# Kernel tuning notes

Measured on AMD Instinct MI355X. Metric: run time of the kernel, lower is better.

## Reference

```python
import jax, jax.numpy as jnp
import numpy as np

HEADS = 8
DIM_HEAD = 32
SCALE = DIM_HEAD ** -0.5


def setup_inputs() -> dict:
    key = jax.random.key(0)
    k1, k2, k3 = jax.random.split(key, 3)
    B, H, W, C = 16, 64, 64, 256
    hidden = HEADS * DIM_HEAD  # 256
    x = jax.random.normal(k1, (B, H, W, C), dtype=jnp.float32)
    # 1x1 convs with no bias == dense matmuls over channel dim (glorot-ish scale)
    w_qkv = jax.random.normal(k2, (C, 3 * hidden), dtype=jnp.float32) * (1.0 / np.sqrt(C))
    w_out = jax.random.normal(k3, (hidden, C), dtype=jnp.float32) * (1.0 / np.sqrt(hidden))
    return {"x": x, "w_qkv": w_qkv, "w_out": w_out}


def reference(x, w_qkv, w_out):
    B, H, W, C = x.shape
    n = H * W
    # to_qkv: 1x1 conv, no bias
    qkv = jnp.einsum('bhwc,cf->bhwf', x, w_qkv)  # [B,H,W,3*hidden]
    q, k, v = jnp.split(qkv, 3, axis=-1)

    def to_heads(t):
        # 'b x y (h c) -> b h c (x y)'
        t = t.reshape(B, n, HEADS, DIM_HEAD)
        return jnp.transpose(t, (0, 2, 3, 1))  # [B, heads, dim_head, n]

    q, k, v = to_heads(q), to_heads(k), to_heads(v)
    q = jax.nn.softmax(q, axis=-2) * SCALE      # softmax over feature dim d
    k = jax.nn.softmax(k, axis=-1)              # softmax over spatial dim n
    context = jnp.einsum('bhdn,bhen->bhde', k, v)   # [B, heads, d, e]
    out = jnp.einsum('bhde,bhdn->bhen', context, q)  # [B, heads, e, n]
    # 'b h c (x y) -> b x y (h c)'
    out = jnp.transpose(out, (0, 3, 1, 2)).reshape(B, H, W, HEADS * DIM_HEAD)
    # to_out: 1x1 conv, no bias
    return jnp.einsum('bhwf,fc->bhwc', out, w_out)
```

## Files before the change

### kernel.cpp

```cpp
#include <hip/hip_runtime.h>

using short8 = __attribute__((ext_vector_type(8))) short;
using f32x4  = __attribute__((ext_vector_type(4))) float;

#define SCALE_Q 0.17677669529663687f
#define NCHUNK 16

__device__ __forceinline__ unsigned short f2bf(float f) {
  unsigned u = __float_as_uint(f);
  return (unsigned short)((u + 0x7FFFu + ((u >> 16) & 1u)) >> 16);
}
__device__ __forceinline__ float bf2f(unsigned h) { return __uint_as_float(h << 16); }

__device__ __forceinline__ void bf8_to_f(uint4 r, float* o) {
  o[0] = bf2f(r.x & 0xffffu); o[1] = bf2f(r.x >> 16);
  o[2] = bf2f(r.y & 0xffffu); o[3] = bf2f(r.y >> 16);
  o[4] = bf2f(r.z & 0xffffu); o[5] = bf2f(r.z >> 16);
  o[6] = bf2f(r.w & 0xffffu); o[7] = bf2f(r.w >> 16);
}
__device__ __forceinline__ unsigned pack2(float a, float b) {
  return (unsigned)f2bf(a) | ((unsigned)f2bf(b) << 16);
}

__global__ __launch_bounds__(256) void prep_kernel(
    const float* __restrict__ x, const float* __restrict__ wqkv, const float* __restrict__ wout,
    unsigned short* __restrict__ xb, unsigned short* __restrict__ wqkvT,
    unsigned short* __restrict__ woutT) {
  const int blk = blockIdx.x;
  if (blk < 16384) {
    const size_t i = ((size_t)blk * 256 + threadIdx.x) * 4;
    const float4 v = *(const float4*)(x + i);
    *(ushort4*)(xb + i) = make_ushort4(f2bf(v.x), f2bf(v.y), f2bf(v.z), f2bf(v.w));
  } else if (blk < 16384 + 768) {
    const int n = blk - 16384, k = threadIdx.x;
    wqkvT[n * 256 + k] = f2bf(wqkv[(size_t)k * 768 + n]);
  } else {
    const int c = blk - 16384 - 768, f = threadIdx.x;
    woutT[c * 256 + f] = f2bf(wout[(size_t)f * 256 + c]);
  }
}

template <typename OutT>
__global__ __launch_bounds__(256) void gemm_bt(
    const unsigned short* __restrict__ A, const unsigned short* __restrict__ BT,
    OutT* __restrict__ D, int M, int N, int K,
    size_t strideA, size_t strideB, size_t strideD) {
  __shared__ unsigned short As[128][40];
  __shared__ unsigned short Bs[128][40];
  const int bn = blockIdx.x, bm = blockIdx.y, bz = blockIdx.z;
  const int tid = threadIdx.x, lane = tid & 63, wid = tid >> 6;
  const int wr = wid >> 1, wc = wid & 1;
  const int fr = lane & 15, fk = (lane >> 4) * 8;
  f32x4 acc[4][4] = {};
  const size_t abase = (size_t)bz * strideA + (size_t)bm * 128 * K;
  const size_t bbase = (size_t)bz * strideB + (size_t)bn * 128 * K;

  for (int kt = 0; kt < K; kt += 32) {
    for (int c = tid; c < 512; c += 256) {
      const int row = c >> 2, kc = (c & 3) * 8;
      *(uint4*)&As[row][kc] = *(const uint4*)(A + abase + (size_t)row * K + kt + kc);
      *(uint4*)&Bs[row][kc] = *(const uint4*)(BT + bbase + (size_t)row * K + kt + kc);
    }
    __syncthreads();
    short8 af[4], bfr[4];
#pragma unroll
    for (int i = 0; i < 4; ++i) {
      af[i]  = *(const short8*)&As[wr * 64 + i * 16 + fr][fk];
      bfr[i] = *(const short8*)&Bs[wc * 64 + i * 16 + fr][fk];
    }
#pragma unroll
    for (int mi = 0; mi < 4; ++mi)
#pragma unroll
      for (int nj = 0; nj < 4; ++nj)
        acc[mi][nj] = __builtin_amdgcn_mfma_f32_16x16x32_bf16(af[mi], bfr[nj], acc[mi][nj], 0, 0, 0);
    __syncthreads();
  }
  const size_t r0 = (size_t)bm * 128 + wr * 64;
  const int c0 = bn * 128 + wc * 64;
  OutT* Dz = D + (size_t)bz * strideD;
#pragma unroll
  for (int mi = 0; mi < 4; ++mi)
#pragma unroll
    for (int nj = 0; nj < 4; ++nj) {
      const int col = c0 + nj * 16 + fr;
#pragma unroll
      for (int r = 0; r < 4; ++r) {
        const size_t row = r0 + mi * 16 + (lane >> 4) * 4 + r;
        const float v = acc[mi][nj][r];
        if constexpr (sizeof(OutT) == 2) Dz[row * N + col] = (OutT)f2bf(v);
        else                             Dz[row * N + col] = v;
      }
    }
}

__global__ __launch_bounds__(256) void ctx_part_kernel(const unsigned short* __restrict__ qkv,
                                                       float* __restrict__ part,
                                                       float* __restrict__ spart) {
  const int blk = blockIdx.x;
  const int bh = blk >> 4, chunk = blk & 15;
  const int b = bh >> 3, h = bh & 7;
  const int tid = threadIdx.x, d = tid & 31, g = tid >> 5;
  const unsigned short* kbase =
      qkv + (size_t)b * 4096 * 768 + 256 + h * 32 + (size_t)chunk * 256 * 768;
  const unsigned short* vbase = kbase + 256;

  __shared__ float ek[64][36], vv[64][36];
  float a0 = 0.f, a1 = 0.f, a2 = 0.f, a3 = 0.f, ssum = 0.f;
  const int e0 = g * 4;
  const int sn = tid >> 2, sc = (tid & 3) * 8;
  const unsigned short* kp0 = kbase + (size_t)sn * 768 + sc;
  const unsigned short* vp0 = vbase + (size_t)sn * 768 + sc;
  uint4 kr = *(const uint4*)kp0;
  uint4 vr = *(const uint4*)vp0;
  for (int n0 = 0; n0 < 256; n0 += 64) {
    float kf[8], vf[8];
    bf8_to_f(kr, kf); bf8_to_f(vr, vf);
    uint4 krn = kr, vrn = vr;
    if (n0 + 64 < 256) {
      krn = *(const uint4*)(kp0 + (size_t)(n0 + 64) * 768);
      vrn = *(const uint4*)(vp0 + (size_t)(n0 + 64) * 768);
    }
#pragma unroll
    for (int j = 0; j < 8; ++j) { ek[sn][sc + j] = __expf(kf[j]); vv[sn][sc + j] = vf[j]; }
    __syncthreads();
#pragma unroll 8
    for (int i = 0; i < 64; ++i) {
      const float kd = ek[i][d];
      const float4 v4 = *(const float4*)&vv[i][e0];
      ssum += kd;
      a0 += kd * v4.x; a1 += kd * v4.y; a2 += kd * v4.z; a3 += kd * v4.w;
    }
    __syncthreads();
    kr = krn; vr = vrn;
  }
  float* pp = part + ((size_t)chunk * 128 + bh) * 1024 + d * 32 + e0;
  pp[0] = a0; pp[1] = a1; pp[2] = a2; pp[3] = a3;
  if (g == 0) spart[((size_t)chunk * 128 + bh) * 32 + d] = ssum;
}

__global__ __launch_bounds__(256) void ctx_combine_kernel(const float* __restrict__ part,
                                                          const float* __restrict__ spart,
                                                          float* __restrict__ ctx) {
  const int bh = blockIdx.x, tid = threadIdx.x;
  __shared__ float sinv[32];
  if (tid < 32) {
    float s = 0.f;
#pragma unroll
    for (int c = 0; c < NCHUNK; ++c) s += spart[((size_t)c * 128 + bh) * 32 + tid];
    sinv[tid] = 1.0f / s;
  }
  __syncthreads();
  float4 acc = make_float4(0.f, 0.f, 0.f, 0.f);
#pragma unroll
  for (int c = 0; c < NCHUNK; ++c) {
    const float4 p = *(const float4*)(part + ((size_t)c * 128 + bh) * 1024 + tid * 4);
    acc.x += p.x; acc.y += p.y; acc.z += p.z; acc.w += p.w;
  }
  const float si = sinv[tid >> 3];
  float4* cp = (float4*)(ctx + (size_t)bh * 1024 + tid * 4);
  *cp = make_float4(acc.x * si, acc.y * si, acc.z * si, acc.w * si);
}

__global__ __launch_bounds__(256) void qsoftmax_kernel(const unsigned short* __restrict__ qkv,
                                                       unsigned short* __restrict__ qs) {
  const size_t t = (size_t)blockIdx.x * 256 + threadIdx.x;
  const size_t n = t >> 3; const int h = (int)(t & 7);
  const unsigned short* qp = qkv + n * 768 + h * 32;
  float q[32];
  bf8_to_f(*(const uint4*)(qp + 0),  q + 0);
  bf8_to_f(*(const uint4*)(qp + 8),  q + 8);
  bf8_to_f(*(const uint4*)(qp + 16), q + 16);
  bf8_to_f(*(const uint4*)(qp + 24), q + 24);
  float mx = q[0];
#pragma unroll
  for (int j = 1; j < 32; ++j) mx = fmaxf(mx, q[j]);
  float ssum = 0.f;
#pragma unroll
  for (int j = 0; j < 32; ++j) { q[j] = __expf(q[j] - mx); ssum += q[j]; }
  const float inv = SCALE_Q / ssum;
  uint4* op = (uint4*)(qs + n * 256 + h * 32);
  op[0] = make_uint4(pack2(q[0]*inv,  q[1]*inv),  pack2(q[2]*inv,  q[3]*inv),
                     pack2(q[4]*inv,  q[5]*inv),  pack2(q[6]*inv,  q[7]*inv));
  op[1] = make_uint4(pack2(q[8]*inv,  q[9]*inv),  pack2(q[10]*inv, q[11]*inv),
                     pack2(q[12]*inv, q[13]*inv), pack2(q[14]*inv, q[15]*inv));
  op[2] = make_uint4(pack2(q[16]*inv, q[17]*inv), pack2(q[18]*inv, q[19]*inv),
                     pack2(q[20]*inv, q[21]*inv), pack2(q[22]*inv, q[23]*inv));
  op[3] = make_uint4(pack2(q[24]*inv, q[25]*inv), pack2(q[26]*inv, q[27]*inv),
                     pack2(q[28]*inv, q[29]*inv), pack2(q[30]*inv, q[31]*inv));
}

__global__ __launch_bounds__(256) void w2_kernel(const float* __restrict__ ctx,
                                                 const unsigned short* __restrict__ woutT,
                                                 unsigned short* __restrict__ W2T) {
  const int b = blockIdx.x >> 4, cg = blockIdx.x & 15;
  const int tid = threadIdx.x;
  __shared__ float cs[8 * 32 * 32];
  {
    const float4* src = (const float4*)(ctx + (size_t)b * 8192);
    float4* dst = (float4*)cs;
#pragma unroll
    for (int i = 0; i < 8; ++i) dst[tid + i * 256] = src[tid + i * 256];
  }
  __syncthreads();
  const int c = cg * 16 + (tid >> 4), chunk = tid & 15;
  const int h = chunk >> 1, d0 = (chunk & 1) * 16;
  float wf[32];
  {
    const uint4* wp = (const uint4*)(woutT + (size_t)c * 256 + h * 32);
    bf8_to_f(wp[0], wf + 0); bf8_to_f(wp[1], wf + 8);
    bf8_to_f(wp[2], wf + 16); bf8_to_f(wp[3], wf + 24);
  }
  unsigned short o[16];
#pragma unroll
  for (int dd = 0; dd < 16; ++dd) {
    const float* cp = cs + h * 1024 + (d0 + dd) * 32;
    float acc = 0.f;
#pragma unroll
    for (int e = 0; e < 32; ++e) acc += cp[e] * wf[e];
    o[dd] = f2bf(acc);
  }
  uint4* op = (uint4*)(W2T + ((size_t)b * 256 + c) * 256 + chunk * 16);
  op[0] = make_uint4((unsigned)o[0] | ((unsigned)o[1] << 16), (unsigned)o[2] | ((unsigned)o[3] << 16),
                     (unsigned)o[4] | ((unsigned)o[5] << 16), (unsigned)o[6] | ((unsigned)o[7] << 16));
  op[1] = make_uint4((unsigned)o[8] | ((unsigned)o[9] << 16), (unsigned)o[10] | ((unsigned)o[11] << 16),
                     (unsigned)o[12] | ((unsigned)o[13] << 16), (unsigned)o[14] | ((unsigned)o[15] << 16));
}

extern "C" void kernel_launch(void* const* d_in, const int* in_sizes, int n_in,
                              void* d_out, int out_size, void* d_ws, size_t ws_size,
                              hipStream_t stream) {
  const float* x     = (const float*)d_in[0];
  const float* wqkv  = (const float*)d_in[1];
  const float* wout  = (const float*)d_in[2];
  float* out = (float*)d_out;

  char* ws = (char*)d_ws;
  unsigned short* xb    = (unsigned short*)(ws);
  unsigned short* wqkvT = (unsigned short*)(ws + 33554432);
  unsigned short* woutT = (unsigned short*)(ws + 33947648);
  unsigned short* qkv   = (unsigned short*)(ws + 34078720);
  float*          ctx   = (float*)        (ws + 134742016);
  unsigned short* qs    = (unsigned short*)(ws + 135266304);
  float*          part  = (float*)(ws);
  float*          spart = (float*)(ws + 8388608);
  unsigned short* W2T   = (unsigned short*)(ws + 12582912);

  prep_kernel<<<16384 + 768 + 256, 256, 0, stream>>>(x, wqkv, wout, xb, wqkvT, woutT);
  gemm_bt<unsigned short><<<dim3(6, 512, 1), 256, 0, stream>>>(
      xb, wqkvT, qkv, 65536, 768, 256, 0, 0, 0);
  ctx_part_kernel<<<2048, 256, 0, stream>>>(qkv, part, spart);
  ctx_combine_kernel<<<128, 256, 0, stream>>>(part, spart, ctx);
  qsoftmax_kernel<<<2048, 256, 0, stream>>>(qkv, qs);
  w2_kernel<<<256, 256, 0, stream>>>(ctx, woutT, W2T);
  gemm_bt<float><<<dim3(2, 32, 16), 256, 0, stream>>>(
      qs, W2T, out, 4096, 256, 256, 4096 * 256, 256 * 256, 4096 * 256);
}
```

Baseline: 184.9 us.

## Fuse Q softmax into QKV GEMM epilogue and use direct global-to-LDS loads

The QKV projection GEMM now applies the per-head feature softmax to the Q columns in its epilogue, using lane shuffles, and writes bf16 Q straight to the qs buffer. The separate qsoftmax kernel is removed, and the intermediate buffer shrinks to K/V only, which saves a write and re-read of Q. The GEMM mainloop now uses global_load_lds with a 64-wide K tile and an unpadded LDS layout, plus a blockwise grid swizzle for better cache locality. The unpadded LDS rows may cause bank conflicts on the fragment reads.

```diff
diff --git a/kernel.cpp b/kernel.cpp
--- a/kernel.cpp
+++ b/kernel.cpp
@@ -18,8 +18,11 @@
   o[4] = bf2f(r.z & 0xffffu); o[5] = bf2f(r.z >> 16);
   o[6] = bf2f(r.w & 0xffffu); o[7] = bf2f(r.w >> 16);
 }
-__device__ __forceinline__ unsigned pack2(float a, float b) {
-  return (unsigned)f2bf(a) | ((unsigned)f2bf(b) << 16);
+
+__device__ __forceinline__ void gl_lds16(const unsigned short* g, unsigned short* l) {
+  __builtin_amdgcn_global_load_lds(
+      (const __attribute__((address_space(1))) void*)g,
+      (__attribute__((address_space(3))) void*)l, 16, 0, 0);
 }
 
 __global__ __launch_bounds__(256) void prep_kernel(
@@ -40,52 +43,92 @@
   }
 }
 
-template <typename OutT>
+template <typename OutT, bool QSOFT, bool SWZ>
 __global__ __launch_bounds__(256) void gemm_bt(
     const unsigned short* __restrict__ A, const unsigned short* __restrict__ BT,
-    OutT* __restrict__ D, int M, int N, int K,
+    OutT* __restrict__ D, unsigned short* __restrict__ QS,
+    int nbn, int K, int N,
     size_t strideA, size_t strideB, size_t strideD) {
-  __shared__ unsigned short As[128][40];
-  __shared__ unsigned short Bs[128][40];
-  const int bn = blockIdx.x, bm = blockIdx.y, bz = blockIdx.z;
+  __shared__ unsigned short As[128 * 64];
+  __shared__ unsigned short Bs[128 * 64];
+  int lin = blockIdx.x;
+  if (SWZ) {
+    const int cpx = gridDim.x >> 3;
+    lin = (lin & 7) * cpx + (lin >> 3);
+  }
+  const int bn = lin % nbn, bm = lin / nbn, bz = blockIdx.z;
   const int tid = threadIdx.x, lane = tid & 63, wid = tid >> 6;
   const int wr = wid >> 1, wc = wid & 1;
-  const int fr = lane & 15, fk = (lane >> 4) * 8;
+  const int fr = lane & 15, hi = lane >> 4;
   f32x4 acc[4][4] = {};
-  const size_t abase = (size_t)bz * strideA + (size_t)bm * 128 * K;
-  const size_t bbase = (size_t)bz * strideB + (size_t)bn * 128 * K;
-
-  for (int kt = 0; kt < K; kt += 32) {
-    for (int c = tid; c < 512; c += 256) {
-      const int row = c >> 2, kc = (c & 3) * 8;
-      *(uint4*)&As[row][kc] = *(const uint4*)(A + abase + (size_t)row * K + kt + kc);
-      *(uint4*)&Bs[row][kc] = *(const uint4*)(BT + bbase + (size_t)row * K + kt + kc);
-    }
-    __syncthreads();
-    short8 af[4], bfr[4];
+  const unsigned short* Ab = A + (size_t)bz * strideA + (size_t)bm * 128 * K;
+  const unsigned short* Bb = BT + (size_t)bz * strideB + (size_t)bn * 128 * K;
+
+  const int srow = wid * 32 + (lane >> 3);
+  const int scol = (lane & 7) * 8;
+  const unsigned short* Ap = Ab + (size_t)srow * K + scol;
+  const unsigned short* Bp = Bb + (size_t)srow * K + scol;
+  unsigned short* Asw = As + (wid * 4) * 512 + 0;
+  unsigned short* Bsw = Bs + (wid * 4) * 512 + 0;
+
+  for (int kt = 0; kt < K; kt += 64) {
 #pragma unroll
     for (int i = 0; i < 4; ++i) {
-      af[i]  = *(const short8*)&As[wr * 64 + i * 16 + fr][fk];
-      bfr[i] = *(const short8*)&Bs[wc * 64 + i * 16 + fr][fk];
-    }
+      gl_lds16(Ap + (size_t)i * 8 * K + kt, Asw + i * 512);
+      gl_lds16(Bp + (size_t)i * 8 * K + kt, Bsw + i * 512);
+    }
+    __syncthreads();
+#pragma unroll
+    for (int kk = 0; kk < 2; ++kk) {
+      short8 af[4], bfv[4];
+#pragma unroll
+      for (int i = 0; i < 4; ++i) {
+        af[i]  = *(const short8*)&As[(wr * 64 + i * 16 + fr) * 64 + kk * 32 + hi * 8];
+        bfv[i] = *(const short8*)&Bs[(wc * 64 + i * 16 + fr) * 64 + kk * 32 + hi * 8];
+      }
+#pragma unroll
+      for (int mi = 0; mi < 4; ++mi)
+#pragma unroll
+        for (int nj = 0; nj < 4; ++nj)
+          acc[mi][nj] = __builtin_amdgcn_mfma_f32_16x16x32_bf16(af[mi], bfv[nj], acc[mi][nj], 0, 0, 0);
+    }
+    __syncthreads();
+  }
+
+  const size_t r0 = (size_t)bm * 128 + wr * 64;
+  if (QSOFT && bn < 2) {
+    const int c0 = bn * 128 + wc * 64;
 #pragma unroll
     for (int mi = 0; mi < 4; ++mi)
 #pragma unroll
-      for (int nj = 0; nj < 4; ++nj)
-        acc[mi][nj] = __builtin_amdgcn_mfma_f32_16x16x32_bf16(af[mi], bfr[nj], acc[mi][nj], 0, 0, 0);
-    __syncthreads();
-  }
-  const size_t r0 = (size_t)bm * 128 + wr * 64;
-  const int c0 = bn * 128 + wc * 64;
+      for (int p = 0; p < 2; ++p)
+#pragma unroll
+        for (int r = 0; r < 4; ++r) {
+          const float v0 = acc[mi][2 * p][r], v1 = acc[mi][2 * p + 1][r];
+          float mx = fmaxf(v0, v1);
+#pragma unroll
+          for (int xm = 1; xm < 16; xm <<= 1) mx = fmaxf(mx, __shfl_xor(mx, xm, 64));
+          const float e0 = __expf(v0 - mx), e1 = __expf(v1 - mx);
+          float s = e0 + e1;
+#pragma unroll
+          for (int xm = 1; xm < 16; xm <<= 1) s += __shfl_xor(s, xm, 64);
+          const float inv = SCALE_Q / s;
+          const size_t row = r0 + mi * 16 + hi * 4 + r;
+          QS[row * 256 + c0 + p * 32 + fr]      = f2bf(e0 * inv);
+          QS[row * 256 + c0 + p * 32 + 16 + fr] = f2bf(e1 * inv);
+        }
+    return;
+  }
+  const int colbase = (QSOFT ? (bn - 2) : bn) * 128 + wc * 64;
   OutT* Dz = D + (size_t)bz * strideD;
 #pragma unroll
   for (int mi = 0; mi < 4; ++mi)
 #pragma unroll
     for (int nj = 0; nj < 4; ++nj) {
-      const int col = c0 + nj * 16 + fr;
+      const int col = colbase + nj * 16 + fr;
 #pragma unroll
       for (int r = 0; r < 4; ++r) {
-        const size_t row = r0 + mi * 16 + (lane >> 4) * 4 + r;
+        const size_t row = r0 + mi * 16 + hi * 4 + r;
         const float v = acc[mi][nj][r];
         if constexpr (sizeof(OutT) == 2) Dz[row * N + col] = (OutT)f2bf(v);
         else                             Dz[row * N + col] = v;
@@ -93,7 +136,7 @@
     }
 }
 
-__global__ __launch_bounds__(256) void ctx_part_kernel(const unsigned short* __restrict__ qkv,
+__global__ __launch_bounds__(256) void ctx_part_kernel(const unsigned short* __restrict__ kv,
                                                        float* __restrict__ part,
                                                        float* __restrict__ spart) {
   const int blk = blockIdx.x;
@@ -101,15 +144,15 @@
   const int b = bh >> 3, h = bh & 7;
   const int tid = threadIdx.x, d = tid & 31, g = tid >> 5;
   const unsigned short* kbase =
-      qkv + (size_t)b * 4096 * 768 + 256 + h * 32 + (size_t)chunk * 256 * 768;
+      kv + (size_t)b * 4096 * 512 + h * 32 + (size_t)chunk * 256 * 512;
   const unsigned short* vbase = kbase + 256;
 
   __shared__ float ek[64][36], vv[64][36];
   float a0 = 0.f, a1 = 0.f, a2 = 0.f, a3 = 0.f, ssum = 0.f;
   const int e0 = g * 4;
   const int sn = tid >> 2, sc = (tid & 3) * 8;
-  const unsigned short* kp0 = kbase + (size_t)sn * 768 + sc;
-  const unsigned short* vp0 = vbase + (size_t)sn * 768 + sc;
+  const unsigned short* kp0 = kbase + (size_t)sn * 512 + sc;
+  const unsigned short* vp0 = vbase + (size_t)sn * 512 + sc;
   uint4 kr = *(const uint4*)kp0;
   uint4 vr = *(const uint4*)vp0;
   for (int n0 = 0; n0 < 256; n0 += 64) {
@@ -117,8 +160,8 @@
     bf8_to_f(kr, kf); bf8_to_f(vr, vf);
     uint4 krn = kr, vrn = vr;
     if (n0 + 64 < 256) {
-      krn = *(const uint4*)(kp0 + (size_t)(n0 + 64) * 768);
-      vrn = *(const uint4*)(vp0 + (size_t)(n0 + 64) * 768);
+      krn = *(const uint4*)(kp0 + (size_t)(n0 + 64) * 512);
+      vrn = *(const uint4*)(vp0 + (size_t)(n0 + 64) * 512);
     }
 #pragma unroll
     for (int j = 0; j < 8; ++j) { ek[sn][sc + j] = __expf(kf[j]); vv[sn][sc + j] = vf[j]; }
@@ -159,34 +202,6 @@
   const float si = sinv[tid >> 3];
   float4* cp = (float4*)(ctx + (size_t)bh * 1024 + tid * 4);
   *cp = make_float4(acc.x * si, acc.y * si, acc.z * si, acc.w * si);
-}
-
-__global__ __launch_bounds__(256) void qsoftmax_kernel(const unsigned short* __restrict__ qkv,
-                                                       unsigned short* __restrict__ qs) {
-  const size_t t = (size_t)blockIdx.x * 256 + threadIdx.x;
-  const size_t n = t >> 3; const int h = (int)(t & 7);
-  const unsigned short* qp = qkv + n * 768 + h * 32;
-  float q[32];
-  bf8_to_f(*(const uint4*)(qp + 0),  q + 0);
-  bf8_to_f(*(const uint4*)(qp + 8),  q + 8);
-  bf8_to_f(*(const uint4*)(qp + 16), q + 16);
-  bf8_to_f(*(const uint4*)(qp + 24), q + 24);
-  float mx = q[0];
-#pragma unroll
-  for (int j = 1; j < 32; ++j) mx = fmaxf(mx, q[j]);
-  float ssum = 0.f;
-#pragma unroll
-  for (int j = 0; j < 32; ++j) { q[j] = __expf(q[j] - mx); ssum += q[j]; }
-  const float inv = SCALE_Q / ssum;
-  uint4* op = (uint4*)(qs + n * 256 + h * 32);
-  op[0] = make_uint4(pack2(q[0]*inv,  q[1]*inv),  pack2(q[2]*inv,  q[3]*inv),
-                     pack2(q[4]*inv,  q[5]*inv),  pack2(q[6]*inv,  q[7]*inv));
-  op[1] = make_uint4(pack2(q[8]*inv,  q[9]*inv),  pack2(q[10]*inv, q[11]*inv),
-                     pack2(q[12]*inv, q[13]*inv), pack2(q[14]*inv, q[15]*inv));
-  op[2] = make_uint4(pack2(q[16]*inv, q[17]*inv), pack2(q[18]*inv, q[19]*inv),
-                     pack2(q[20]*inv, q[21]*inv), pack2(q[22]*inv, q[23]*inv));
-  op[3] = make_uint4(pack2(q[24]*inv, q[25]*inv), pack2(q[26]*inv, q[27]*inv),
-                     pack2(q[28]*inv, q[29]*inv), pack2(q[30]*inv, q[31]*inv));
 }
 
 __global__ __launch_bounds__(256) void w2_kernel(const float* __restrict__ ctx,
@@ -238,20 +253,19 @@
   unsigned short* xb    = (unsigned short*)(ws);
   unsigned short* wqkvT = (unsigned short*)(ws + 33554432);
   unsigned short* woutT = (unsigned short*)(ws + 33947648);
-  unsigned short* qkv   = (unsigned short*)(ws + 34078720);
-  float*          ctx   = (float*)        (ws + 134742016);
-  unsigned short* qs    = (unsigned short*)(ws + 135266304);
+  unsigned short* kv    = (unsigned short*)(ws + 34078720);
+  float*          ctx   = (float*)        (ws + 101187584);
+  unsigned short* qs    = (unsigned short*)(ws + 101711872);
   float*          part  = (float*)(ws);
   float*          spart = (float*)(ws + 8388608);
   unsigned short* W2T   = (unsigned short*)(ws + 12582912);
 
   prep_kernel<<<16384 + 768 + 256, 256, 0, stream>>>(x, wqkv, wout, xb, wqkvT, woutT);
-  gemm_bt<unsigned short><<<dim3(6, 512, 1), 256, 0, stream>>>(
-      xb, wqkvT, qkv, 65536, 768, 256, 0, 0, 0);
-  ctx_part_kernel<<<2048, 256, 0, stream>>>(qkv, part, spart);
+  gemm_bt<unsigned short, true, true><<<3072, 256, 0, stream>>>(
+      xb, wqkvT, kv, qs, 6, 256, 512, 0, 0, 0);
+  ctx_part_kernel<<<2048, 256, 0, stream>>>(kv, part, spart);
   ctx_combine_kernel<<<128, 256, 0, stream>>>(part, spart, ctx);
-  qsoftmax_kernel<<<2048, 256, 0, stream>>>(qkv, qs);
   w2_kernel<<<256, 256, 0, stream>>>(ctx, woutT, W2T);
-  gemm_bt<float><<<dim3(2, 32, 16), 256, 0, stream>>>(
-      qs, W2T, out, 4096, 256, 256, 4096 * 256, 256 * 256, 4096 * 256);
-}
+  gemm_bt<float, false, false><<<dim3(64, 1, 16), 256, 0, stream>>>(
+      qs, W2T, out, nullptr, 2, 256, 256, (size_t)4096 * 256, (size_t)256 * 256, (size_t)4096 * 256);
+}
```

After: 175.0 us. 5.4% less time.
